# Kernel optimization log

Hardware: AMD Instinct MI355X
Metric: run time of the kernel (lower is better)

The kernel has to match this reference:

```python
import jax, jax.numpy as jnp
import numpy as np
import math

B, S, E, H = 4, 2048, 512, 8
DK = E // H
NEG = -1000000000.0


def setup_inputs() -> dict:
    key = jax.random.key(0)
    ks = jax.random.split(key, 12)
    std = 1.0 / math.sqrt(E)
    inp = {
        "query": jax.random.normal(ks[0], (B, S, E), dtype=jnp.float32),
        "key_in": jax.random.normal(ks[1], (B, S, E), dtype=jnp.float32),
        "value": jax.random.normal(ks[2], (B, S, E), dtype=jnp.float32),
        "mask": jax.random.randint(ks[3], (B, S, S), 0, 2, dtype=jnp.int32),
        "Wq": jax.random.normal(ks[4], (E, E), dtype=jnp.float32) * std,
        "bq": jnp.zeros((E,), dtype=jnp.float32),
        "Wk": jax.random.normal(ks[5], (E, E), dtype=jnp.float32) * std,
        "bk": jnp.zeros((E,), dtype=jnp.float32),
        "Wv": jax.random.normal(ks[6], (E, E), dtype=jnp.float32) * std,
        "bv": jnp.zeros((E,), dtype=jnp.float32),
        "Wo": jax.random.normal(ks[7], (E, E), dtype=jnp.float32) * std,
        "bo": jnp.zeros((E,), dtype=jnp.float32),
    }
    return inp


def reference(query, key_in, value, mask, Wq, bq, Wk, bk, Wv, bv, Wo, bo):
    # Linear projections (torch nn.Linear: x @ W.T + b)
    q = (query @ Wq.T + bq).reshape(B, S, H, DK).transpose(0, 2, 1, 3)   # [B,H,S,dk]
    k = (key_in @ Wk.T + bk).reshape(B, S, H, DK).transpose(0, 2, 1, 3)
    v = (value @ Wv.T + bv).reshape(B, S, H, DK).transpose(0, 2, 1, 3)
    # Faithful quirk: scores MULTIPLIED by sqrt(dk), as in the source
    scores = jnp.einsum("bhqd,bhkd->bhqk", q, k) * math.sqrt(DK)
    scores = jnp.where(mask[:, None, :, :] == 0, NEG, scores)
    attn = jax.nn.softmax(scores, axis=-1)
    out = jnp.einsum("bhqk,bhkd->bhqd", attn, v)                         # [B,H,S,dk]
    # Faithful quirk: direct view [B,H,S,dk] -> [B,S,E] WITHOUT head transpose
    out = out.reshape(B, S, E)
    return out @ Wo.T + bo
```

## Files before the change

kernel.cpp:

```cpp
#include <hip/hip_runtime.h>

#define BB 4
#define SS 2048
#define EE 512
#define HH 8
#define DKK 64
#define MM (BB*SS)

typedef unsigned short u16;
typedef unsigned int u32;
typedef unsigned long long u64;
typedef __attribute__((ext_vector_type(8))) short short8;
typedef __attribute__((ext_vector_type(4))) short short4v;
typedef __attribute__((ext_vector_type(4))) float f32x4;

__device__ inline u16 f2bf(float f) {
  union { float f; u32 u; } v; v.f = f;
  u32 r = v.u + 0x7fff + ((v.u >> 16) & 1);
  return (u16)(r >> 16);
}
__device__ inline float bf2f(u16 u) {
  union { u32 u; float f; } v; v.u = ((u32)u) << 16;
  return v.f;
}
__device__ inline void split2(float f, u16 &h, u16 &l) {
  h = f2bf(f);
  l = f2bf(f - bf2f(h));
}

__global__ __launch_bounds__(256) void maskpack(const int* __restrict__ mask,
                                                u64* __restrict__ mb) {
  const int bq = blockIdx.x;
  const int w = threadIdx.x >> 6, l = threadIdx.x & 63;
  const int* src = mask + (size_t)bq * SS;
  #pragma unroll
  for (int it = 0; it < 8; ++it) {
    int tb = it * 4 + w;
    int m = src[tb * 64 + l];
    u64 bits = __ballot(m != 0);
    if (l == 0) mb[(size_t)bq * 32 + tb] = bits;
  }
}

template<int COMP>
__global__ __launch_bounds__(256) void proj(
    const float* __restrict__ A, const float* __restrict__ W,
    const float* __restrict__ bias, u16* __restrict__ Chi, u16* __restrict__ Clo,
    float cscale)
{
  __shared__ __align__(16) u16 Ah[128][72];
  __shared__ __align__(16) u16 Al[COMP ? 128 : 1][72];
  __shared__ __align__(16) u16 Bh[64][72];
  __shared__ __align__(16) u16 Bl[COMP ? 64 : 1][72];
  const int m0 = blockIdx.x * 128, n0 = blockIdx.y * 64;
  const int tid = threadIdx.x, w = tid >> 6, l = tid & 63;
  const int row = l & 15, kq = (l >> 4) * 8;
  f32x4 acc[2][4];
  #pragma unroll
  for (int i = 0; i < 2; ++i)
    #pragma unroll
    for (int j = 0; j < 4; ++j) acc[i][j] = (f32x4){0.f, 0.f, 0.f, 0.f};

  for (int k0 = 0; k0 < 512; k0 += 64) {
    __syncthreads();
    #pragma unroll
    for (int i = 0; i < 8; ++i) {
      int u = tid + i * 256; int r = u >> 4, c4 = (u & 15) * 4;
      f32x4 v = *(const f32x4*)&A[(size_t)(m0 + r) * 512 + k0 + c4];
      u16 h[4], lo[4];
      #pragma unroll
      for (int j = 0; j < 4; ++j) split2(v[j], h[j], lo[j]);
      *(short4v*)&Ah[r][c4] = (short4v){(short)h[0], (short)h[1], (short)h[2], (short)h[3]};
      if (COMP)
        *(short4v*)&Al[r][c4] = (short4v){(short)lo[0], (short)lo[1], (short)lo[2], (short)lo[3]};
    }
    #pragma unroll
    for (int i = 0; i < 4; ++i) {
      int u = tid + i * 256; int r = u >> 4, c4 = (u & 15) * 4;
      f32x4 v = *(const f32x4*)&W[(size_t)(n0 + r) * 512 + k0 + c4];
      u16 h[4], lo[4];
      #pragma unroll
      for (int j = 0; j < 4; ++j) split2(v[j], h[j], lo[j]);
      *(short4v*)&Bh[r][c4] = (short4v){(short)h[0], (short)h[1], (short)h[2], (short)h[3]};
      if (COMP)
        *(short4v*)&Bl[r][c4] = (short4v){(short)lo[0], (short)lo[1], (short)lo[2], (short)lo[3]};
    }
    __syncthreads();
    short8 ah[2][2], al[2][2], bh[4][2], bl[4][2];
    #pragma unroll
    for (int mf = 0; mf < 2; ++mf)
      #pragma unroll
      for (int ks = 0; ks < 2; ++ks) {
        ah[mf][ks] = *(const short8*)&Ah[w * 32 + mf * 16 + row][ks * 32 + kq];
        if (COMP) al[mf][ks] = *(const short8*)&Al[w * 32 + mf * 16 + row][ks * 32 + kq];
      }
    #pragma unroll
    for (int nf = 0; nf < 4; ++nf)
      #pragma unroll
      for (int ks = 0; ks < 2; ++ks) {
        bh[nf][ks] = *(const short8*)&Bh[nf * 16 + row][ks * 32 + kq];
        if (COMP) bl[nf][ks] = *(const short8*)&Bl[nf * 16 + row][ks * 32 + kq];
      }
    #pragma unroll
    for (int mf = 0; mf < 2; ++mf)
      #pragma unroll
      for (int nf = 0; nf < 4; ++nf)
        #pragma unroll
        for (int ks = 0; ks < 2; ++ks) {
          acc[mf][nf] = __builtin_amdgcn_mfma_f32_16x16x32_bf16(
              ah[mf][ks], bh[nf][ks], acc[mf][nf], 0, 0, 0);
          if (COMP) {
            acc[mf][nf] = __builtin_amdgcn_mfma_f32_16x16x32_bf16(
                ah[mf][ks], bl[nf][ks], acc[mf][nf], 0, 0, 0);
            acc[mf][nf] = __builtin_amdgcn_mfma_f32_16x16x32_bf16(
                al[mf][ks], bh[nf][ks], acc[mf][nf], 0, 0, 0);
          }
        }
  }
  #pragma unroll
  for (int mf = 0; mf < 2; ++mf)
    #pragma unroll
    for (int nf = 0; nf < 4; ++nf)
      #pragma unroll
      for (int r = 0; r < 4; ++r) {
        int m = m0 + w * 32 + mf * 16 + ((l >> 4) << 2) + r;
        int n = n0 + nf * 16 + (l & 15);
        float c = (acc[mf][nf][r] + bias[n]) * cscale;
        size_t idx = (size_t)m * 512 + n;
        if (COMP) { u16 h, lo; split2(c, h, lo); Chi[idx] = h; Clo[idx] = lo; }
        else Chi[idx] = f2bf(c);
      }
}

__global__ __launch_bounds__(256) void gemm_out(
    const u16* __restrict__ A, const float* __restrict__ W,
    const float* __restrict__ bias, float* __restrict__ C)
{
  __shared__ __align__(16) u16 As[128][72];
  __shared__ __align__(16) u16 Bs[64][72];
  const int m0 = blockIdx.x * 128, n0 = blockIdx.y * 64;
  const int tid = threadIdx.x, w = tid >> 6, l = tid & 63;
  const int row = l & 15, kq = (l >> 4) * 8;
  f32x4 acc[2][4];
  #pragma unroll
  for (int i = 0; i < 2; ++i)
    #pragma unroll
    for (int j = 0; j < 4; ++j) acc[i][j] = (f32x4){0.f, 0.f, 0.f, 0.f};

  for (int k0 = 0; k0 < 512; k0 += 64) {
    __syncthreads();
    #pragma unroll
    for (int i = 0; i < 4; ++i) {
      int u = tid + i * 256; int r = u >> 3, c = (u & 7) * 8;
      *(short8*)&As[r][c] = *(const short8*)&A[(size_t)(m0 + r) * 512 + k0 + c];
    }
    #pragma unroll
    for (int i = 0; i < 4; ++i) {
      int u = tid + i * 256; int r = u >> 4, c4 = (u & 15) * 4;
      f32x4 v = *(const f32x4*)&W[(size_t)(n0 + r) * 512 + k0 + c4];
      *(short4v*)&Bs[r][c4] = (short4v){(short)f2bf(v[0]), (short)f2bf(v[1]),
                                        (short)f2bf(v[2]), (short)f2bf(v[3])};
    }
    __syncthreads();
    short8 a[2][2], bfr[4][2];
    #pragma unroll
    for (int mf = 0; mf < 2; ++mf)
      #pragma unroll
      for (int ks = 0; ks < 2; ++ks)
        a[mf][ks] = *(const short8*)&As[w * 32 + mf * 16 + row][ks * 32 + kq];
    #pragma unroll
    for (int nf = 0; nf < 4; ++nf)
      #pragma unroll
      for (int ks = 0; ks < 2; ++ks)
        bfr[nf][ks] = *(const short8*)&Bs[nf * 16 + row][ks * 32 + kq];
    #pragma unroll
    for (int mf = 0; mf < 2; ++mf)
      #pragma unroll
      for (int nf = 0; nf < 4; ++nf)
        #pragma unroll
        for (int ks = 0; ks < 2; ++ks)
          acc[mf][nf] = __builtin_amdgcn_mfma_f32_16x16x32_bf16(
              a[mf][ks], bfr[nf][ks], acc[mf][nf], 0, 0, 0);
  }
  #pragma unroll
  for (int mf = 0; mf < 2; ++mf)
    #pragma unroll
    for (int nf = 0; nf < 4; ++nf)
      #pragma unroll
      for (int r = 0; r < 4; ++r) {
        int m = m0 + w * 32 + mf * 16 + ((l >> 4) << 2) + r;
        int n = n0 + nf * 16 + (l & 15);
        C[(size_t)m * 512 + n] = acc[mf][nf][r] + bias[n];
      }
}

__global__ __launch_bounds__(256) void attn(
    const u16* __restrict__ Qhi, const u16* __restrict__ Qlo,
    const u16* __restrict__ Khi, const u16* __restrict__ Klo,
    const u16* __restrict__ V, const u64* __restrict__ MB,
    u16* __restrict__ X)
{
  __shared__ __align__(16) u16 KhiS[64][64];
  __shared__ __align__(16) u16 KloS[64][64];
  __shared__ __align__(16) u16 VtS[64][64];
  __shared__ __align__(16) u16 Pl[64][64];
  const int b = blockIdx.z, h = blockIdx.y, q0 = blockIdx.x * 64;
  const int tid = threadIdx.x, w = tid >> 6, l = tid & 63;
  const int row = l & 15, kq = (l >> 4) * 8;

  const size_t qbase = ((size_t)(b * SS) + q0 + w * 16 + row) * EE + h * DKK;
  short8 qh[2], ql[2];
  #pragma unroll
  for (int ks = 0; ks < 2; ++ks) {
    qh[ks] = *(const short8*)&Qhi[qbase + ks * 32 + kq];
    ql[ks] = *(const short8*)&Qlo[qbase + ks * 32 + kq];
  }

  float mrow[4], lrow[4];
  f32x4 acco[4];
  #pragma unroll
  for (int r = 0; r < 4; ++r) { mrow[r] = -INFINITY; lrow[r] = 0.f; }
  #pragma unroll
  for (int f = 0; f < 4; ++f) acco[f] = (f32x4){0.f, 0.f, 0.f, 0.f};

  const int qr0 = q0 + w * 16 + ((l >> 4) << 2);

  for (int t0 = 0; t0 < SS; t0 += 64) {
    __syncthreads();
    #pragma unroll
    for (int i = 0; i < 2; ++i) {
      int u = tid + i * 256; int r = u >> 3, c0 = (u & 7) * 8;
      size_t g = ((size_t)(b * SS) + t0 + r) * EE + h * DKK + c0;
      short8 hv = *(const short8*)&Khi[g];
      short8 lv = *(const short8*)&Klo[g];
      short8 vv = *(const short8*)&V[g];
      *(short8*)&KhiS[r][c0] = hv;
      *(short8*)&KloS[r][c0] = lv;
      int tswz = r ^ c0;
      #pragma unroll
      for (int j = 0; j < 8; ++j) VtS[c0 + j][tswz] = (u16)vv[j];
    }
    __syncthreads();

    u64 wb[4];
    #pragma unroll
    for (int r = 0; r < 4; ++r)
      wb[r] = MB[((size_t)(b * SS) + qr0 + r) * 32 + (t0 >> 6)] >> (l & 15);

    f32x4 sacc[4];
    #pragma unroll
    for (int f = 0; f < 4; ++f) sacc[f] = (f32x4){0.f, 0.f, 0.f, 0.f};
    #pragma unroll
    for (int f = 0; f < 4; ++f)
      #pragma unroll
      for (int ks = 0; ks < 2; ++ks) {
        short8 kh = *(const short8*)&KhiS[f * 16 + row][ks * 32 + kq];
        short8 kl = *(const short8*)&KloS[f * 16 + row][ks * 32 + kq];
        sacc[f] = __builtin_amdgcn_mfma_f32_16x16x32_bf16(qh[ks], kh, sacc[f], 0, 0, 0);
        sacc[f] = __builtin_amdgcn_mfma_f32_16x16x32_bf16(qh[ks], kl, sacc[f], 0, 0, 0);
        sacc[f] = __builtin_amdgcn_mfma_f32_16x16x32_bf16(ql[ks], kh, sacc[f], 0, 0, 0);
      }

    float sval[4][4];
    #pragma unroll
    for (int f = 0; f < 4; ++f)
      #pragma unroll
      for (int r = 0; r < 4; ++r)
        sval[f][r] = ((wb[r] >> (16 * f)) & 1ULL) ? sacc[f][r] : -1e9f;

    #pragma unroll
    for (int r = 0; r < 4; ++r) {
      float mx = fmaxf(fmaxf(sval[0][r], sval[1][r]), fmaxf(sval[2][r], sval[3][r]));
      #pragma unroll
      for (int off = 1; off < 16; off <<= 1) mx = fmaxf(mx, __shfl_xor(mx, off));
      float mnew = fmaxf(mrow[r], mx);
      float alpha = __expf(mrow[r] - mnew);
      float rs = 0.f;
      #pragma unroll
      for (int f = 0; f < 4; ++f) {
        float p = __expf(sval[f][r] - mnew);
        sval[f][r] = p; rs += p;
      }
      #pragma unroll
      for (int off = 1; off < 16; off <<= 1) rs += __shfl_xor(rs, off);
      lrow[r] = lrow[r] * alpha + rs;
      mrow[r] = mnew;
      #pragma unroll
      for (int f = 0; f < 4; ++f) acco[f][r] *= alpha;
    }

    #pragma unroll
    for (int f = 0; f < 4; ++f)
      #pragma unroll
      for (int r = 0; r < 4; ++r) {
        int rr = ((l >> 4) << 2) + r;
        Pl[w * 16 + rr][(f * 16 + (l & 15)) ^ ((rr & 7) << 3)] = f2bf(sval[f][r]);
      }

    #pragma unroll
    for (int f2 = 0; f2 < 4; ++f2) {
      int d = f2 * 16 + row;
      int vswz = d & 56;
      #pragma unroll
      for (int ks = 0; ks < 2; ++ks) {
        short8 p = *(const short8*)&Pl[w * 16 + row][(ks * 32 + kq) ^ ((row & 7) << 3)];
        short8 vvf = *(const short8*)&VtS[d][(ks * 32 + kq) ^ vswz];
        acco[f2] = __builtin_amdgcn_mfma_f32_16x16x32_bf16(p, vvf, acco[f2], 0, 0, 0);
      }
    }
  }

  #pragma unroll
  for (int f2 = 0; f2 < 4; ++f2)
    #pragma unroll
    for (int r = 0; r < 4; ++r) {
      int q = q0 + w * 16 + ((l >> 4) << 2) + r;
      int d = f2 * 16 + (l & 15);
      float o = acco[f2][r] / lrow[r];
      int sp = h * 256 + (q >> 3);
      int ep = ((q & 7) << 6) + d;
      X[((size_t)(b * SS) + sp) * EE + ep] = f2bf(o);
    }
}

extern "C" void kernel_launch(void* const* d_in, const int* in_sizes, int n_in,
                              void* d_out, int out_size, void* d_ws, size_t ws_size,
                              hipStream_t stream) {
  const float* query  = (const float*)d_in[0];
  const float* key_in = (const float*)d_in[1];
  const float* value  = (const float*)d_in[2];
  const int*   mask   = (const int*)d_in[3];
  const float* Wq = (const float*)d_in[4];
  const float* bq = (const float*)d_in[5];
  const float* Wk = (const float*)d_in[6];
  const float* bk = (const float*)d_in[7];
  const float* Wv = (const float*)d_in[8];
  const float* bv = (const float*)d_in[9];
  const float* Wo = (const float*)d_in[10];
  const float* bo = (const float*)d_in[11];

  u16* ws = (u16*)d_ws;
  const size_t NE = (size_t)MM * EE;
  u16* Qhi = ws;
  u16* Qlo = ws + NE;
  u16* Khi = ws + 2 * NE;
  u16* Klo = ws + 3 * NE;
  u16* Vp  = ws + 4 * NE;
  u16* X   = ws + 5 * NE;
  u64* MBb = (u64*)(ws + 6 * NE);

  dim3 gblk(MM / 128, EE / 64);
  maskpack<<<MM, 256, 0, stream>>>(mask, MBb);
  proj<1><<<gblk, 256, 0, stream>>>(query,  Wq, bq, Qhi, Qlo, 8.0f);
  proj<1><<<gblk, 256, 0, stream>>>(key_in, Wk, bk, Khi, Klo, 1.0f);
  proj<0><<<gblk, 256, 0, stream>>>(value,  Wv, bv, Vp, nullptr, 1.0f);
  attn<<<dim3(SS / 64, HH, BB), 256, 0, stream>>>(Qhi, Qlo, Khi, Klo, Vp, MBb, X);
  gemm_out<<<gblk, 256, 0, stream>>>(X, Wo, bo, (float*)d_out);
}
```

Before: 437.6 us.

## Prefetch next K/V tile into registers, swizzle LDS layouts, use DPP row reductions

```diff
diff --git a/kernel.cpp b/kernel.cpp
--- a/kernel.cpp
+++ b/kernel.cpp
@@ -26,6 +26,26 @@
 __device__ inline void split2(float f, u16 &h, u16 &l) {
   h = f2bf(f);
   l = f2bf(f - bf2f(h));
+}
+
+template<int CTRL>
+__device__ inline float fdpp(float x) {
+  return __builtin_bit_cast(float,
+      __builtin_amdgcn_update_dpp(0, __builtin_bit_cast(int, x), CTRL, 0xf, 0xf, true));
+}
+__device__ inline float rmax16(float x) {
+  x = fmaxf(x, fdpp<0x121>(x));
+  x = fmaxf(x, fdpp<0x122>(x));
+  x = fmaxf(x, fdpp<0x124>(x));
+  x = fmaxf(x, fdpp<0x128>(x));
+  return x;
+}
+__device__ inline float rsum16(float x) {
+  x += fdpp<0x121>(x);
+  x += fdpp<0x122>(x);
+  x += fdpp<0x124>(x);
+  x += fdpp<0x128>(x);
+  return x;
 }
 
 __global__ __launch_bounds__(256) void maskpack(const int* __restrict__ mask,
@@ -207,6 +227,8 @@
   const int b = blockIdx.z, h = blockIdx.y, q0 = blockIdx.x * 64;
   const int tid = threadIdx.x, w = tid >> 6, l = tid & 63;
   const int row = l & 15, kq = (l >> 4) * 8;
+  const int r0 = tid >> 3;
+  const int c0 = (tid & 7) * 8;
 
   const size_t qbase = ((size_t)(b * SS) + q0 + w * 16 + row) * EE + h * DKK;
   short8 qh[2], ql[2];
@@ -224,42 +246,65 @@
   for (int f = 0; f < 4; ++f) acco[f] = (f32x4){0.f, 0.f, 0.f, 0.f};
 
   const int qr0 = q0 + w * 16 + ((l >> 4) << 2);
+  const size_t mbase = ((size_t)(b * SS) + qr0) * 32;
+
+  short8 sh[2], sl[2], sv[2];
+  u64 wb[4], wbn[4];
+
+  #pragma unroll
+  for (int i = 0; i < 2; ++i) {
+    size_t g = ((size_t)(b * SS) + r0 + 32 * i) * EE + h * DKK + c0;
+    sh[i] = *(const short8*)&Khi[g];
+    sl[i] = *(const short8*)&Klo[g];
+    sv[i] = *(const short8*)&V[g];
+  }
+  #pragma unroll
+  for (int r = 0; r < 4; ++r) wb[r] = MB[mbase + r * 32] >> (l & 15);
+  #pragma unroll
+  for (int i = 0; i < 2; ++i) {
+    int rr = r0 + 32 * i;
+    int kc = c0 ^ ((rr & 7) << 3);
+    *(short8*)&KhiS[rr][kc] = sh[i];
+    *(short8*)&KloS[rr][kc] = sl[i];
+    #pragma unroll
+    for (int j = 0; j < 8; ++j) {
+      int d = c0 + j;
+      VtS[d][rr ^ (((d & 7) ^ (d >> 3)) << 3)] = (u16)sv[i][j];
+    }
+  }
+  __syncthreads();
 
   for (int t0 = 0; t0 < SS; t0 += 64) {
-    __syncthreads();
-    #pragma unroll
-    for (int i = 0; i < 2; ++i) {
-      int u = tid + i * 256; int r = u >> 3, c0 = (u & 7) * 8;
-      size_t g = ((size_t)(b * SS) + t0 + r) * EE + h * DKK + c0;
-      short8 hv = *(const short8*)&Khi[g];
-      short8 lv = *(const short8*)&Klo[g];
-      short8 vv = *(const short8*)&V[g];
-      *(short8*)&KhiS[r][c0] = hv;
-      *(short8*)&KloS[r][c0] = lv;
-      int tswz = r ^ c0;
-      #pragma unroll
-      for (int j = 0; j < 8; ++j) VtS[c0 + j][tswz] = (u16)vv[j];
-    }
-    __syncthreads();
-
-    u64 wb[4];
-    #pragma unroll
-    for (int r = 0; r < 4; ++r)
-      wb[r] = MB[((size_t)(b * SS) + qr0 + r) * 32 + (t0 >> 6)] >> (l & 15);
+    const bool more = (t0 + 64 < SS);
+    if (more) {
+      #pragma unroll
+      for (int i = 0; i < 2; ++i) {
+        size_t g = ((size_t)(b * SS) + t0 + 64 + r0 + 32 * i) * EE + h * DKK + c0;
+        sh[i] = *(const short8*)&Khi[g];
+        sl[i] = *(const short8*)&Klo[g];
+        sv[i] = *(const short8*)&V[g];
+      }
+      #pragma unroll
+      for (int r = 0; r < 4; ++r)
+        wbn[r] = MB[mbase + r * 32 + ((t0 >> 6) + 1)] >> (l & 15);
+    }
 
     f32x4 sacc[4];
     #pragma unroll
     for (int f = 0; f < 4; ++f) sacc[f] = (f32x4){0.f, 0.f, 0.f, 0.f};
     #pragma unroll
-    for (int f = 0; f < 4; ++f)
+    for (int f = 0; f < 4; ++f) {
+      int krow = f * 16 + row;
+      int ksw = (krow & 7) << 3;
       #pragma unroll
       for (int ks = 0; ks < 2; ++ks) {
-        short8 kh = *(const short8*)&KhiS[f * 16 + row][ks * 32 + kq];
-        short8 kl = *(const short8*)&KloS[f * 16 + row][ks * 32 + kq];
+        short8 kh = *(const short8*)&KhiS[krow][(ks * 32 + kq) ^ ksw];
+        short8 kl = *(const short8*)&KloS[krow][(ks * 32 + kq) ^ ksw];
         sacc[f] = __builtin_amdgcn_mfma_f32_16x16x32_bf16(qh[ks], kh, sacc[f], 0, 0, 0);
         sacc[f] = __builtin_amdgcn_mfma_f32_16x16x32_bf16(qh[ks], kl, sacc[f], 0, 0, 0);
         sacc[f] = __builtin_amdgcn_mfma_f32_16x16x32_bf16(ql[ks], kh, sacc[f], 0, 0, 0);
       }
+    }
 
     float sval[4][4];
     #pragma unroll
@@ -271,8 +316,7 @@
     #pragma unroll
     for (int r = 0; r < 4; ++r) {
       float mx = fmaxf(fmaxf(sval[0][r], sval[1][r]), fmaxf(sval[2][r], sval[3][r]));
-      #pragma unroll
-      for (int off = 1; off < 16; off <<= 1) mx = fmaxf(mx, __shfl_xor(mx, off));
+      mx = rmax16(mx);
       float mnew = fmaxf(mrow[r], mx);
       float alpha = __expf(mrow[r] - mnew);
       float rs = 0.f;
@@ -281,8 +325,7 @@
         float p = __expf(sval[f][r] - mnew);
         sval[f][r] = p; rs += p;
       }
-      #pragma unroll
-      for (int off = 1; off < 16; off <<= 1) rs += __shfl_xor(rs, off);
+      rs = rsum16(rs);
       lrow[r] = lrow[r] * alpha + rs;
       mrow[r] = mnew;
       #pragma unroll
@@ -294,20 +337,42 @@
       #pragma unroll
       for (int r = 0; r < 4; ++r) {
         int rr = ((l >> 4) << 2) + r;
-        Pl[w * 16 + rr][(f * 16 + (l & 15)) ^ ((rr & 7) << 3)] = f2bf(sval[f][r]);
-      }
-
-    #pragma unroll
-    for (int f2 = 0; f2 < 4; ++f2) {
-      int d = f2 * 16 + row;
-      int vswz = d & 56;
-      #pragma unroll
-      for (int ks = 0; ks < 2; ++ks) {
-        short8 p = *(const short8*)&Pl[w * 16 + row][(ks * 32 + kq) ^ ((row & 7) << 3)];
-        short8 vvf = *(const short8*)&VtS[d][(ks * 32 + kq) ^ vswz];
-        acco[f2] = __builtin_amdgcn_mfma_f32_16x16x32_bf16(p, vvf, acco[f2], 0, 0, 0);
-      }
-    }
+        Pl[w * 16 + rr][(f * 16 + (l & 15)) ^ (((rr & 7) ^ (rr >> 3)) << 3)] = f2bf(sval[f][r]);
+      }
+
+    {
+      int psw = ((row & 7) ^ (row >> 3)) << 3;
+      #pragma unroll
+      for (int f2 = 0; f2 < 4; ++f2) {
+        int d = f2 * 16 + row;
+        int vsw = ((d & 7) ^ (d >> 3)) << 3;
+        #pragma unroll
+        for (int ks = 0; ks < 2; ++ks) {
+          short8 p = *(const short8*)&Pl[w * 16 + row][(ks * 32 + kq) ^ psw];
+          short8 vvf = *(const short8*)&VtS[d][(ks * 32 + kq) ^ vsw];
+          acco[f2] = __builtin_amdgcn_mfma_f32_16x16x32_bf16(p, vvf, acco[f2], 0, 0, 0);
+        }
+      }
+    }
+
+    __syncthreads();
+    if (more) {
+      #pragma unroll
+      for (int i = 0; i < 2; ++i) {
+        int rr = r0 + 32 * i;
+        int kc = c0 ^ ((rr & 7) << 3);
+        *(short8*)&KhiS[rr][kc] = sh[i];
+        *(short8*)&KloS[rr][kc] = sl[i];
+        #pragma unroll
+        for (int j = 0; j < 8; ++j) {
+          int d = c0 + j;
+          VtS[d][rr ^ (((d & 7) ^ (d >> 3)) << 3)] = (u16)sv[i][j];
+        }
+      }
+      #pragma unroll
+      for (int r = 0; r < 4; ++r) wb[r] = wbn[r];
+    }
+    __syncthreads();
   }
 
   #pragma unroll
```

New measurement: 394.1 us. 9.9% less time.
